# Kernel optimization log

Hardware: AMD Instinct MI355X
Metric: run time of the kernel (lower is better)

The kernel has to match this reference:

```python
import jax, jax.numpy as jnp
import numpy as np

N = 100000   # nodes
E = 800000   # directed edges (before self-loops)
D = 64       # hidden_dim
NUM_ROUNDS = 4
EPS = 1e-5


def setup_inputs() -> dict:
    key = jax.random.key(0)
    k0, k1, k2 = jax.random.split(key, 3)
    x = jax.random.normal(k0, (N, D), dtype=jnp.float32)
    edge_index = jax.random.randint(k1, (2, E), 0, N, dtype=jnp.int32)
    W = jax.random.normal(k2, (D, D), dtype=jnp.float32) * (1.0 / np.sqrt(D))
    b = jnp.zeros((D,), dtype=jnp.float32)
    gamma = jnp.ones((D,), dtype=jnp.float32)
    beta = jnp.zeros((D,), dtype=jnp.float32)
    return {"x": x, "edge_index": edge_index, "W": W, "b": b,
            "gamma": gamma, "beta": beta, "num_rounds": NUM_ROUNDS}


def reference(x, edge_index, W, b, gamma, beta, num_rounds):
    n = x.shape[0]
    # GCNConv: add self-loops, symmetric degree normalization D^-1/2 (A+I) D^-1/2
    loops = jnp.arange(n, dtype=edge_index.dtype)
    src = jnp.concatenate([edge_index[0], loops])  # [E+N] message sources
    dst = jnp.concatenate([edge_index[1], loops])  # [E+N] message targets
    deg = jax.ops.segment_sum(jnp.ones_like(dst, dtype=x.dtype), dst, num_segments=n)
    dis = jnp.where(deg > 0, jax.lax.rsqrt(deg), 0.0)  # deg^-1/2, 0 for isolated
    norm = dis[src] * dis[dst]                          # [E+N] edge weights

    for _ in range(num_rounds):
        h = x @ W                                                      # [N, D]
        msgs = h[src] * norm[:, None]                                  # gather [E+N, D]
        agg = jax.ops.segment_sum(msgs, dst, num_segments=n) + b      # scatter-add
        # LayerNorm over feature dim
        mu = agg.mean(axis=-1, keepdims=True)
        var = agg.var(axis=-1, keepdims=True)
        x = (agg - mu) * jax.lax.rsqrt(var + EPS) * gamma + beta
    return x
```

## Files before the change

### kernel.cpp

```cpp
#include <hip/hip_runtime.h>

#define D 64
#define EPSV 1e-5f
#define SLOTMAX 40

typedef _Float16 f16;
typedef _Float16 f16x8 __attribute__((ext_vector_type(8)));
typedef float f32x4 __attribute__((ext_vector_type(4)));


__global__ void k_init(int* cursor, int n) {
    int i = blockIdx.x * blockDim.x + threadIdx.x;
    if (i < n) cursor[i] = 0;
}

__global__ void k_fill(const int* __restrict__ src, const int* __restrict__ dst,
                       int* __restrict__ cursor, unsigned* __restrict__ slots, int e) {
    int i = blockIdx.x * blockDim.x + threadIdx.x;
    if (i >= e) return;
    int s_ = src[i], d_ = dst[i];
    int p = atomicAdd(&cursor[d_], 1);
    slots[(size_t)d_ * SLOTMAX + p] = (unsigned)s_;
}

__global__ void k_dis(const int* __restrict__ cursor, float* __restrict__ disv, int n) {
    int i = blockIdx.x * blockDim.x + threadIdx.x;
    if (i < n) disv[i] = rsqrtf((float)(cursor[i] + 1));
}

__global__ void k_wpack(const float* __restrict__ W, f16* __restrict__ Wp) {
    int idx = blockIdx.x * blockDim.x + threadIdx.x;
    if (idx >= 512) return;
    int s = idx >> 8, rem = idx & 255, t = rem >> 6, l = rem & 63;
    int q = l >> 4, c = l & 15;
#pragma unroll
    for (int j = 0; j < 8; ++j) {
        int k = 32 * s + 8 * q + j;
        Wp[(size_t)idx * 8 + j] = (f16)W[k * D + 16 * t + c];
    }
}

__global__ __launch_bounds__(256) void k_xform(
    const float* __restrict__ x, const f16* __restrict__ Wp,
    const float* __restrict__ disv, f16* __restrict__ h, int n, int ntiles) {
    const int wv = blockIdx.x * 4 + (threadIdx.x >> 6);
    const int lane = threadIdx.x & 63;
    const int q = lane >> 4, c = lane & 15;

    const f16x8* wp = (const f16x8*)Wp;
    f16x8 w0 = wp[0 * 64 + lane], w1 = wp[1 * 64 + lane];
    f16x8 w2 = wp[2 * 64 + lane], w3 = wp[3 * 64 + lane];
    f16x8 w4 = wp[4 * 64 + lane], w5 = wp[5 * 64 + lane];
    f16x8 w6 = wp[6 * 64 + lane], w7 = wp[7 * 64 + lane];

#pragma unroll
    for (int tt = 0; tt < 2; ++tt) {
        const int tile = wv * 2 + tt;
        if (tile >= ntiles) break;
        const int row0 = tile * 16;
        const int rA = (row0 + c < n) ? (row0 + c) : (n - 1);

        const float4* xr = (const float4*)(x + (size_t)rA * D);
        float4 u0 = xr[2 * q], u1 = xr[2 * q + 1];
        float4 u2 = xr[8 + 2 * q], u3 = xr[9 + 2 * q];
        f16x8 a0 = (f16x8){(f16)u0.x, (f16)u0.y, (f16)u0.z, (f16)u0.w,
                           (f16)u1.x, (f16)u1.y, (f16)u1.z, (f16)u1.w};
        f16x8 a1 = (f16x8){(f16)u2.x, (f16)u2.y, (f16)u2.z, (f16)u2.w,
                           (f16)u3.x, (f16)u3.y, (f16)u3.z, (f16)u3.w};

        f32x4 d0 = {0,0,0,0}, d1 = {0,0,0,0}, d2 = {0,0,0,0}, d3 = {0,0,0,0};
        d0 = __builtin_amdgcn_mfma_f32_16x16x32_f16(a0, w0, d0, 0, 0, 0);
        d1 = __builtin_amdgcn_mfma_f32_16x16x32_f16(a0, w1, d1, 0, 0, 0);
        d2 = __builtin_amdgcn_mfma_f32_16x16x32_f16(a0, w2, d2, 0, 0, 0);
        d3 = __builtin_amdgcn_mfma_f32_16x16x32_f16(a0, w3, d3, 0, 0, 0);
        d0 = __builtin_amdgcn_mfma_f32_16x16x32_f16(a1, w4, d0, 0, 0, 0);
        d1 = __builtin_amdgcn_mfma_f32_16x16x32_f16(a1, w5, d1, 0, 0, 0);
        d2 = __builtin_amdgcn_mfma_f32_16x16x32_f16(a1, w6, d2, 0, 0, 0);
        d3 = __builtin_amdgcn_mfma_f32_16x16x32_f16(a1, w7, d3, 0, 0, 0);

        f32x4 dvv = *(const f32x4*)(disv + row0 + 4 * q);
#pragma unroll
        for (int r = 0; r < 4; ++r) {
            int row = row0 + q * 4 + r;
            if (row < n) {
                f16* hr = h + (size_t)row * D + c;
                hr[0]  = (f16)(d0[r] * dvv[r]);
                hr[16] = (f16)(d1[r] * dvv[r]);
                hr[32] = (f16)(d2[r] * dvv[r]);
                hr[48] = (f16)(d3[r] * dvv[r]);
            }
        }
    }
}

template<bool LAST>
__global__ __launch_bounds__(256) void k_fuse(
    const f16* __restrict__ h, const unsigned* __restrict__ slots,
    const int* __restrict__ cursor, const float* __restrict__ disv,
    const float* __restrict__ bb, const float* __restrict__ gamma,
    const float* __restrict__ beta, const f16* __restrict__ Wp,
    float* __restrict__ out, f16* __restrict__ hnext, int n) {
    __shared__ __align__(16) f16 ylds[32][72];

    const int tid = threadIdx.x;
    const int grp = tid >> 3;
    const int fl  = tid & 7;
    const int w = blockIdx.x * 32 + grp;
    const bool act = (w < n);

    if (act) {
        const int jb = w * SLOTMAX;
        const int dg = cursor[w];

        float acc[8];
        {
            f16x8 sv = *(const f16x8*)(h + (size_t)w * D + fl * 8);
#pragma unroll
            for (int f = 0; f < 8; ++f) acc[f] = (float)sv[f];
        }

        uint4 s0 = *(const uint4*)(slots + jb);
        uint4 s1 = *(const uint4*)(slots + jb + 4);
        uint4 s2 = *(const uint4*)(slots + jb + 8);
        const unsigned idx[12] = {s0.x, s0.y, s0.z, s0.w,
                                  s1.x, s1.y, s1.z, s1.w,
                                  s2.x, s2.y, s2.z, s2.w};
        f16x8 v[12];
#pragma unroll
        for (int k = 0; k < 12; ++k) {
            unsigned u = (k < dg) ? idx[k] : 0u;
            v[k] = *(const f16x8*)(h + (size_t)u * D + fl * 8);
        }
#pragma unroll
        for (int k = 0; k < 12; ++k) {
            float m = (k < dg) ? 1.0f : 0.0f;
#pragma unroll
            for (int f = 0; f < 8; ++f) acc[f] += m * (float)v[k][f];
        }
        int j = 12;
        while (j < dg) {
            uint4 sr = *(const uint4*)(slots + jb + j);
            const unsigned uu[4] = {sr.x, sr.y, sr.z, sr.w};
#pragma unroll
            for (int k = 0; k < 4; ++k) {
                unsigned u = (j + k < dg) ? uu[k] : 0u;
                float m = (j + k < dg) ? 1.0f : 0.0f;
                f16x8 vv = *(const f16x8*)(h + (size_t)u * D + fl * 8);
#pragma unroll
                for (int f = 0; f < 8; ++f) acc[f] += m * (float)vv[f];
            }
            j += 4;
        }

        const float dv = disv[w];
        const float4 b0 = ((const float4*)bb)[fl * 2],    b1 = ((const float4*)bb)[fl * 2 + 1];
        const float4 g0 = ((const float4*)gamma)[fl * 2], g1 = ((const float4*)gamma)[fl * 2 + 1];
        const float4 e0 = ((const float4*)beta)[fl * 2],  e1 = ((const float4*)beta)[fl * 2 + 1];
        const float bs[8] = {b0.x, b0.y, b0.z, b0.w, b1.x, b1.y, b1.z, b1.w};
        const float gs[8] = {g0.x, g0.y, g0.z, g0.w, g1.x, g1.y, g1.z, g1.w};
        const float es[8] = {e0.x, e0.y, e0.z, e0.w, e1.x, e1.y, e1.z, e1.w};

#pragma unroll
        for (int f = 0; f < 8; ++f) acc[f] = acc[f] * dv + bs[f];

        float s = 0.0f;
#pragma unroll
        for (int f = 0; f < 8; ++f) s += acc[f];
#pragma unroll
        for (int m = 1; m < 8; m <<= 1) s += __shfl_xor(s, m);
        float mu = s * (1.0f / 64.0f);
        float dd[8], qv = 0.0f;
#pragma unroll
        for (int f = 0; f < 8; ++f) { dd[f] = acc[f] - mu; qv += dd[f] * dd[f]; }
#pragma unroll
        for (int m = 1; m < 8; m <<= 1) qv += __shfl_xor(qv, m);
        float rstd = rsqrtf(qv * (1.0f / 64.0f) + EPSV);

        if (LAST) {
            float4 o0, o1;
            o0.x = dd[0] * rstd * gs[0] + es[0]; o0.y = dd[1] * rstd * gs[1] + es[1];
            o0.z = dd[2] * rstd * gs[2] + es[2]; o0.w = dd[3] * rstd * gs[3] + es[3];
            o1.x = dd[4] * rstd * gs[4] + es[4]; o1.y = dd[5] * rstd * gs[5] + es[5];
            o1.z = dd[6] * rstd * gs[6] + es[6]; o1.w = dd[7] * rstd * gs[7] + es[7];
            float4* orow = (float4*)(out + (size_t)w * D);
            orow[fl * 2] = o0; orow[fl * 2 + 1] = o1;
        } else {
            f16x8 yv;
#pragma unroll
            for (int f = 0; f < 8; ++f) yv[f] = (f16)(dd[f] * rstd * gs[f] + es[f]);
            *(f16x8*)(&ylds[grp][fl * 8]) = yv;
        }
    }
    if (LAST) return;

    __syncthreads();

    const int wv = tid >> 6;
    const int lane = tid & 63;
    const int q = lane >> 4, c = lane & 15;

    const f16x8* wp = (const f16x8*)Wp;
    f16x8 wlo = wp[wv * 64 + lane];
    f16x8 whi = wp[(4 + wv) * 64 + lane];

    const int row0 = blockIdx.x * 32;
#pragma unroll
    for (int rt = 0; rt < 2; ++rt) {
        f16x8 a0 = *(const f16x8*)(&ylds[rt * 16 + c][q * 8]);
        f16x8 a1 = *(const f16x8*)(&ylds[rt * 16 + c][32 + q * 8]);
        f32x4 d = {0, 0, 0, 0};
        d = __builtin_amdgcn_mfma_f32_16x16x32_f16(a0, wlo, d, 0, 0, 0);
        d = __builtin_amdgcn_mfma_f32_16x16x32_f16(a1, whi, d, 0, 0, 0);

        const int rbase = row0 + rt * 16;
        f32x4 dvv = *(const f32x4*)(disv + rbase + 4 * q);
#pragma unroll
        for (int r = 0; r < 4; ++r) {
            int row = rbase + q * 4 + r;
            if (row < n)
                hnext[(size_t)row * D + wv * 16 + c] = (f16)(d[r] * dvv[r]);
        }
    }
}


extern "C" void kernel_launch(void* const* d_in, const int* in_sizes, int n_in,
                              void* d_out, int out_size, void* d_ws, size_t ws_size,
                              hipStream_t stream) {
    const float* x0    = (const float*)d_in[0];
    const int*   ei    = (const int*)d_in[1];
    const float* W     = (const float*)d_in[2];
    const float* b     = (const float*)d_in[3];
    const float* gamma = (const float*)d_in[4];
    const float* beta  = (const float*)d_in[5];

    const int N = in_sizes[0] / D;
    const int E = in_sizes[1] / 2;
    const int* src = ei;
    const int* dst = ei + E;

    char* ws = (char*)d_ws;
    size_t off = 0;
    auto alloc = [&](size_t bytes) {
        off = (off + 255) & ~(size_t)255;
        void* p = ws + off;
        off += bytes;
        return p;
    };
    int*      cursor = (int*)alloc((size_t)N * 4);
    unsigned* slots  = (unsigned*)alloc((size_t)N * SLOTMAX * 4);
    float*    disv   = (float*)alloc((size_t)(N + 32) * 4);
    f16*      Wp     = (f16*)alloc(512 * 8 * 2);
    f16*      hA     = (f16*)alloc((size_t)N * D * 2);
    f16*      hB     = (f16*)alloc((size_t)N * D * 2);
    (void)ws_size;

    const int nbN = (N + 255) / 256;
    const int nbE = (E + 255) / 256;

    k_init<<<nbN, 256, 0, stream>>>(cursor, N);
    k_fill<<<nbE, 256, 0, stream>>>(src, dst, cursor, slots, E);
    k_dis <<<nbN, 256, 0, stream>>>(cursor, disv, N);
    k_wpack<<<2, 256, 0, stream>>>(W, Wp);

    float* out = (float*)d_out;
    const int ntiles = (N + 15) / 16;
    const int nwav   = (ntiles + 1) / 2;
    const int GX = (nwav + 3) / 4;
    const int GG = (N + 31) / 32;

    k_xform<<<GX, 256, 0, stream>>>(x0, Wp, disv, hA, N, ntiles);
    k_fuse<false><<<GG, 256, 0, stream>>>(hA, slots, cursor, disv, b, gamma, beta,
                                          Wp, nullptr, hB, N);
    k_fuse<false><<<GG, 256, 0, stream>>>(hB, slots, cursor, disv, b, gamma, beta,
                                          Wp, nullptr, hA, N);
    k_fuse<false><<<GG, 256, 0, stream>>>(hA, slots, cursor, disv, b, gamma, beta,
                                          Wp, nullptr, hB, N);
    k_fuse<true><<<GG, 256, 0, stream>>>(hB, slots, cursor, disv, b, gamma, beta,
                                         Wp, out, nullptr, N);
}
```

Baseline: 242.7 us.

## Shrink per-node adjacency slots to 16 with global overflow edge list

Each node now gets 16 fixed neighbor slots instead of 40. Edges beyond that go into a global (dst, src) overflow list, filled through an atomic counter. The fill kernel now handles four edges per thread. This shrinks the slot array and the fixed-capacity slot reads in the aggregation kernel. The cost is that every high-degree node linearly scans the whole overflow list in every round, which can create a long tail. Overflow beyond the cap is silently dropped.

After: 405.4 us. 1.67x slower.

```diff
diff --git a/kernel.cpp b/kernel.cpp
--- a/kernel.cpp
+++ b/kernel.cpp
@@ -2,25 +2,45 @@
 
 #define D 64
 #define EPSV 1e-5f
-#define SLOTMAX 40
+#define SLOTP 16
+#define OVFCAP 65536
 
 typedef _Float16 f16;
 typedef _Float16 f16x8 __attribute__((ext_vector_type(8)));
 typedef float f32x4 __attribute__((ext_vector_type(4)));
 
 
-__global__ void k_init(int* cursor, int n) {
+__global__ void k_init(int* cursor, int* ocnt, int n) {
     int i = blockIdx.x * blockDim.x + threadIdx.x;
     if (i < n) cursor[i] = 0;
+    if (i == 0) *ocnt = 0;
 }
 
 __global__ void k_fill(const int* __restrict__ src, const int* __restrict__ dst,
-                       int* __restrict__ cursor, unsigned* __restrict__ slots, int e) {
-    int i = blockIdx.x * blockDim.x + threadIdx.x;
-    if (i >= e) return;
-    int s_ = src[i], d_ = dst[i];
-    int p = atomicAdd(&cursor[d_], 1);
-    slots[(size_t)d_ * SLOTMAX + p] = (unsigned)s_;
+                       int* __restrict__ cursor, unsigned* __restrict__ slots,
+                       uint2* __restrict__ ovf, int* __restrict__ ocnt, int e) {
+    const int t = blockIdx.x * blockDim.x + threadIdx.x;
+    const int stride = gridDim.x * blockDim.x;
+    int sv[4], dv[4]; bool ok[4];
+#pragma unroll
+    for (int k = 0; k < 4; ++k) {
+        int i = t + k * stride;
+        ok[k] = (i < e);
+        int ii = ok[k] ? i : 0;
+        sv[k] = src[ii]; dv[k] = dst[ii];
+    }
+#pragma unroll
+    for (int k = 0; k < 4; ++k) {
+        if (!ok[k]) continue;
+        int d_ = dv[k];
+        int p = atomicAdd(&cursor[d_], 1);
+        if (p < SLOTP) {
+            slots[(size_t)d_ * SLOTP + p] = (unsigned)sv[k];
+        } else {
+            int o = atomicAdd(ocnt, 1);
+            if (o < OVFCAP) ovf[o] = uint2{(unsigned)d_, (unsigned)sv[k]};
+        }
+    }
 }
 
 __global__ void k_dis(const int* __restrict__ cursor, float* __restrict__ disv, int n) {
@@ -99,6 +119,7 @@
     const int* __restrict__ cursor, const float* __restrict__ disv,
     const float* __restrict__ bb, const float* __restrict__ gamma,
     const float* __restrict__ beta, const f16* __restrict__ Wp,
+    const uint2* __restrict__ ovf, const int* __restrict__ ocnt,
     float* __restrict__ out, f16* __restrict__ hnext, int n) {
     __shared__ __align__(16) f16 ylds[32][72];
 
@@ -109,8 +130,9 @@
     const bool act = (w < n);
 
     if (act) {
-        const int jb = w * SLOTMAX;
+        const int jb = w * SLOTP;
         const int dg = cursor[w];
+        const int dgp = (dg < SLOTP) ? dg : SLOTP;
 
         float acc[8];
         {
@@ -137,19 +159,28 @@
 #pragma unroll
             for (int f = 0; f < 8; ++f) acc[f] += m * (float)v[k][f];
         }
-        int j = 12;
-        while (j < dg) {
-            uint4 sr = *(const uint4*)(slots + jb + j);
+        if (dgp > 12) {
+            uint4 sr = *(const uint4*)(slots + jb + 12);
             const unsigned uu[4] = {sr.x, sr.y, sr.z, sr.w};
 #pragma unroll
             for (int k = 0; k < 4; ++k) {
-                unsigned u = (j + k < dg) ? uu[k] : 0u;
-                float m = (j + k < dg) ? 1.0f : 0.0f;
+                unsigned u = (12 + k < dgp) ? uu[k] : 0u;
+                float m = (12 + k < dgp) ? 1.0f : 0.0f;
                 f16x8 vv = *(const f16x8*)(h + (size_t)u * D + fl * 8);
 #pragma unroll
                 for (int f = 0; f < 8; ++f) acc[f] += m * (float)vv[f];
             }
-            j += 4;
+        }
+        if (dg > SLOTP) {
+            int oc = *ocnt;
+            for (int i = 0; i < oc; ++i) {
+                uint2 pr = ovf[i];
+                if (pr.x == (unsigned)w) {
+                    f16x8 vv = *(const f16x8*)(h + (size_t)pr.y * D + fl * 8);
+#pragma unroll
+                    for (int f = 0; f < 8; ++f) acc[f] += (float)vv[f];
+                }
+            }
         }
 
         const float dv = disv[w];
@@ -248,7 +279,9 @@
         return p;
     };
     int*      cursor = (int*)alloc((size_t)N * 4);
-    unsigned* slots  = (unsigned*)alloc((size_t)N * SLOTMAX * 4);
+    unsigned* slots  = (unsigned*)alloc((size_t)N * SLOTP * 4);
+    uint2*    ovf    = (uint2*)alloc((size_t)OVFCAP * 8);
+    int*      ocnt   = (int*)alloc(256);
     float*    disv   = (float*)alloc((size_t)(N + 32) * 4);
     f16*      Wp     = (f16*)alloc(512 * 8 * 2);
     f16*      hA     = (f16*)alloc((size_t)N * D * 2);
@@ -256,10 +289,10 @@
     (void)ws_size;
 
     const int nbN = (N + 255) / 256;
-    const int nbE = (E + 255) / 256;
-
-    k_init<<<nbN, 256, 0, stream>>>(cursor, N);
-    k_fill<<<nbE, 256, 0, stream>>>(src, dst, cursor, slots, E);
+    const int nbF = (E + 1023) / 1024;
+
+    k_init<<<nbN, 256, 0, stream>>>(cursor, ocnt, N);
+    k_fill<<<nbF, 256, 0, stream>>>(src, dst, cursor, slots, ovf, ocnt, E);
     k_dis <<<nbN, 256, 0, stream>>>(cursor, disv, N);
     k_wpack<<<2, 256, 0, stream>>>(W, Wp);
 
@@ -271,11 +304,11 @@
 
     k_xform<<<GX, 256, 0, stream>>>(x0, Wp, disv, hA, N, ntiles);
     k_fuse<false><<<GG, 256, 0, stream>>>(hA, slots, cursor, disv, b, gamma, beta,
-                                          Wp, nullptr, hB, N);
+                                          Wp, ovf, ocnt, nullptr, hB, N);
     k_fuse<false><<<GG, 256, 0, stream>>>(hB, slots, cursor, disv, b, gamma, beta,
-                                          Wp, nullptr, hA, N);
+                                          Wp, ovf, ocnt, nullptr, hA, N);
     k_fuse<false><<<GG, 256, 0, stream>>>(hA, slots, cursor, disv, b, gamma, beta,
-                                          Wp, nullptr, hB, N);
+                                          Wp, ovf, ocnt, nullptr, hB, N);
     k_fuse<true><<<GG, 256, 0, stream>>>(hB, slots, cursor, disv, b, gamma, beta,
-                                         Wp, out, nullptr, N);
-}
+                                         Wp, ovf, ocnt, out, nullptr, N);
+}
```
